# Kernel tuning notes

Hardware: AMD Instinct MI355X
Metric: run time of the kernel (lower is better)

The kernel has to match this reference:

```python
import jax, jax.numpy as jnp
import numpy as np

B, S, D, H = 2, 2048, 1024, 16
DH = D // H
DFF = 4 * D
EPS = 1e-5


def layernorm(x, g, b):
    mu = jnp.mean(x, axis=-1, keepdims=True)
    var = jnp.mean(jnp.square(x - mu), axis=-1, keepdims=True)
    return (x - mu) * jax.lax.rsqrt(var + EPS) * g + b


def setup_inputs() -> dict:
    key = jax.random.key(0)
    ks = jax.random.split(key, 12)
    s = 0.02
    return {
        "x": jax.random.normal(ks[0], (B, S, D), dtype=jnp.float32),
        "ln1_g": jnp.ones((D,), jnp.float32),
        "ln1_b": jnp.zeros((D,), jnp.float32),
        "Wq": jax.random.normal(ks[1], (D, D), jnp.float32) * s,
        "bq": jnp.zeros((D,), jnp.float32),
        "Wk": jax.random.normal(ks[2], (D, D), jnp.float32) * s,
        "bk": jnp.zeros((D,), jnp.float32),
        "Wv": jax.random.normal(ks[3], (D, D), jnp.float32) * s,
        "bv": jnp.zeros((D,), jnp.float32),
        "Wo": jax.random.normal(ks[4], (D, D), jnp.float32) * s,
        "bo": jnp.zeros((D,), jnp.float32),
        "ln2_g": jnp.ones((D,), jnp.float32),
        "ln2_b": jnp.zeros((D,), jnp.float32),
        "W1": jax.random.normal(ks[5], (D, DFF), jnp.float32) * s,
        "b1": jnp.zeros((DFF,), jnp.float32),
        "W2": jax.random.normal(ks[6], (DFF, D), jnp.float32) * s,
        "b2": jnp.zeros((D,), jnp.float32),
    }


def block(x, ln1_g, ln1_b, Wq, bq, Wk, bk, Wv, bv, Wo, bo, ln2_g, ln2_b, W1, b1, W2, b2):
    h = layernorm(x, ln1_g, ln1_b)
    # projections -> [B, H, S, DH]
    q = (h @ Wq + bq).reshape(B, S, H, DH).transpose(0, 2, 1, 3)
    k = (h @ Wk + bk).reshape(B, S, H, DH).transpose(0, 2, 1, 3)
    v = (h @ Wv + bv).reshape(B, S, H, DH).transpose(0, 2, 1, 3)
    scores = jnp.einsum('bhqd,bhkd->bhqk', q, k) / jnp.sqrt(jnp.float32(DH))
    causal = jnp.tril(jnp.ones((S, S), dtype=bool))  # True = keep
    scores = jnp.where(causal, scores, -jnp.inf)
    attn = jax.nn.softmax(scores, axis=-1)
    out = jnp.einsum('bhqk,bhkd->bhqd', attn, v)
    out = out.transpose(0, 2, 1, 3).reshape(B, S, D)
    x = x + out @ Wo + bo
    h2 = layernorm(x, ln2_g, ln2_b)
    ff = jax.nn.gelu(h2 @ W1 + b1, approximate=False) @ W2 + b2
    return x + ff


def reference(x, ln1_g, ln1_b, Wq, bq, Wk, bk, Wv, bv, Wo, bo, ln2_g, ln2_b, W1, b1, W2, b2):
    return block(x, ln1_g, ln1_b, Wq, bq, Wk, bk, Wv, bv, Wo, bo, ln2_g, ln2_b, W1, b1, W2, b2)
```

## Files before the change

### kernel.cpp

```cpp
#include <hip/hip_runtime.h>
#include <cstdint>
#include <cstddef>


#define DEV static __device__ __forceinline__

typedef unsigned short u16;
typedef __bf16 bf16x8 __attribute__((ext_vector_type(8)));
typedef u16    u16x8  __attribute__((ext_vector_type(8)));
typedef u16    u16x4  __attribute__((ext_vector_type(4)));
typedef float  f32x4  __attribute__((ext_vector_type(4)));

#define AEXP2(x) __builtin_amdgcn_exp2f(x)

DEV u16 f2bf(float f) {
  unsigned u = __builtin_bit_cast(unsigned, f);
  u += 0x7fffu + ((u >> 16) & 1u);
  return (u16)(u >> 16);
}
DEV u16 f2bfh(float f) {
  return __builtin_bit_cast(u16, (__bf16)f);
}

DEV void gl16(const void* g, void* l) {
  __builtin_amdgcn_global_load_lds(
      (const __attribute__((address_space(1))) unsigned*)g,
      (__attribute__((address_space(3))) unsigned*)l, 16, 0, 0);
}

__global__ __launch_bounds__(256)
void tconv(const float* __restrict__ in, u16* __restrict__ out, int R, int C)
{
  __shared__ float tile[32][33];
  const int tx = threadIdx.x & 31, ty = threadIdx.x >> 5;
  const int r0 = blockIdx.y * 32, c0 = blockIdx.x * 32;
#pragma unroll
  for (int i = 0; i < 4; ++i)
    tile[ty + 8*i][tx] = in[(size_t)(r0 + ty + 8*i) * C + c0 + tx];
  __syncthreads();
#pragma unroll
  for (int i = 0; i < 4; ++i)
    out[(size_t)(c0 + ty + 8*i) * R + r0 + tx] = f2bfh(tile[tx][ty + 8*i]);
}

__global__ __launch_bounds__(256)
void tconv4(const float* __restrict__ w0, const float* __restrict__ w1,
            const float* __restrict__ w2, const float* __restrict__ w3,
            u16* __restrict__ q0, u16* __restrict__ q1,
            u16* __restrict__ q2, u16* __restrict__ q3)
{
  __shared__ float tile[32][33];
  const int z = blockIdx.z;
  const float* in = z == 0 ? w0 : z == 1 ? w1 : z == 2 ? w2 : w3;
  u16* out       = z == 0 ? q0 : z == 1 ? q1 : z == 2 ? q2 : q3;
  const int tx = threadIdx.x & 31, ty = threadIdx.x >> 5;
  const int r0 = blockIdx.y * 32, c0 = blockIdx.x * 32;
#pragma unroll
  for (int i = 0; i < 4; ++i)
    tile[ty + 8*i][tx] = in[(size_t)(r0 + ty + 8*i) * 1024 + c0 + tx];
  __syncthreads();
#pragma unroll
  for (int i = 0; i < 4; ++i)
    out[(size_t)(c0 + ty + 8*i) * 1024 + r0 + tx] = f2bfh(tile[tx][ty + 8*i]);
}

__global__ __launch_bounds__(256)
void ln_fwd(const float* __restrict__ x, const float* __restrict__ g,
            const float* __restrict__ b, u16* __restrict__ out)
{
  const int row = blockIdx.x, t = threadIdx.x;
  const float4 v = ((const float4*)(x + (size_t)row * 1024))[t];
  float s1 = v.x + v.y + v.z + v.w;
  float s2 = v.x*v.x + v.y*v.y + v.z*v.z + v.w*v.w;
#pragma unroll
  for (int d = 1; d < 64; d <<= 1) {
    s1 += __shfl_xor(s1, d, 64);
    s2 += __shfl_xor(s2, d, 64);
  }
  __shared__ float sh[8];
  const int w = t >> 6;
  if ((t & 63) == 0) { sh[w] = s1; sh[w + 4] = s2; }
  __syncthreads();
  s1 = sh[0] + sh[1] + sh[2] + sh[3];
  s2 = sh[4] + sh[5] + sh[6] + sh[7];
  const float mu  = s1 * (1.0f / 1024.0f);
  const float var = s2 * (1.0f / 1024.0f) - mu * mu;
  const float rs  = rsqrtf(var + 1e-5f);
  const float4 gv = ((const float4*)g)[t];
  const float4 bv = ((const float4*)b)[t];
  u16x4 o;
  o[0] = f2bfh((v.x - mu) * rs * gv.x + bv.x);
  o[1] = f2bfh((v.y - mu) * rs * gv.y + bv.y);
  o[2] = f2bfh((v.z - mu) * rs * gv.z + bv.z);
  o[3] = f2bfh((v.w - mu) * rs * gv.w + bv.w);
  *(u16x4*)(out + (size_t)row * 1024 + t * 4) = o;
}

#define EPI_QKV  0
#define EPI_RES  1
#define EPI_GELU 2

#define QSCALE 0.180421f

template<int EPI, int BM, int PIPE, int CM>
__global__ __launch_bounds__(256)
void gemm_bt(const u16* __restrict__ A, const u16* __restrict__ Bt,
             const float* __restrict__ b0, const float* __restrict__ b1,
             const float* __restrict__ b2, const float* __restrict__ res,
             float* __restrict__ outf, u16* __restrict__ o0,
             u16* __restrict__ o1, u16* __restrict__ o2,
             int N, int K)
{
  constexpr int MI = BM / 32;
  constexpr int RA = BM / 32;
  constexpr int NB = PIPE == 2 ? 3 : (PIPE == 1 ? 2 : 1);
  static_assert(PIPE != 2 || BM == 64,  "vmcnt(6) assumes 6 loads/step");
  static_assert(PIPE != 1 || BM == 128, "vmcnt(8) assumes 8 loads/step");
  __shared__ u16 As[NB][BM * 64];
  __shared__ u16 Bs[NB][128 * 64];
  const int t = threadIdx.x, lane = t & 63, w = t >> 6;
  const int wr = w >> 1, wc = w & 1;
  const int d = blockIdx.x + gridDim.x * blockIdx.y;
  const int rr = d >> 3;
  const int m0 = ((d & 7) * CM + rr % CM) * BM;
  const int n0 = (rr / CM) * 128;
  const int li = lane & 15, lg = lane >> 4;

  const int srow = t >> 3;
  const int schunk = (t & 7) ^ (srow & 7);
  const u16* Ag = A  + (size_t)(m0 + srow) * K + schunk * 8;
  const u16* Bg = Bt + (size_t)(n0 + srow) * K + schunk * 8;

  auto STG = [&](int k0, int b) {
#pragma unroll
    for (int p = 0; p < RA; ++p)
      gl16(Ag + k0 + (size_t)(p * 32) * K, &As[b][t * 8 + p * 2048]);
#pragma unroll
    for (int p = 0; p < 4; ++p)
      gl16(Bg + k0 + (size_t)(p * 32) * K, &Bs[b][t * 8 + p * 2048]);
  };

  f32x4 acc[MI][4] = {};
  const int swz = (li & 7) << 4;

  auto COMPUTE = [&](int cur) {
#pragma unroll
    for (int ks = 0; ks < 2; ++ks) {
      bf16x8 af[MI], bfr[4];
#pragma unroll
      for (int i = 0; i < MI; ++i) {
        const int Ra = wr * (MI * 16) + i * 16 + li;
        af[i] = *(const bf16x8*)((const char*)As[cur] + Ra * 128 +
                                 ((ks * 64 + lg * 16) ^ swz));
      }
#pragma unroll
      for (int i = 0; i < 4; ++i) {
        const int Rb = wc * 64 + i * 16 + li;
        bfr[i] = *(const bf16x8*)((const char*)Bs[cur] + Rb * 128 +
                                  ((ks * 64 + lg * 16) ^ swz));
      }
#pragma unroll
      for (int mi = 0; mi < MI; ++mi)
#pragma unroll
        for (int ni = 0; ni < 4; ++ni)
          acc[mi][ni] = __builtin_amdgcn_mfma_f32_16x16x32_bf16(
              af[mi], bfr[ni], acc[mi][ni], 0, 0, 0);
    }
  };

  if (PIPE == 2) {
    STG(0, 0);
    if (64 < K) STG(64, 1);
    int cur = 0;
    for (int k0 = 0; k0 < K; k0 += 64) {
      if (k0 + 64 < K)
        asm volatile("s_waitcnt vmcnt(6)" ::: "memory");
      else
        asm volatile("s_waitcnt vmcnt(0)" ::: "memory");
      __builtin_amdgcn_s_barrier();
      __builtin_amdgcn_sched_barrier(0);
      COMPUTE(cur);
      if (k0 + 128 < K) {
        int nxt = cur + 2; if (nxt >= 3) nxt -= 3;
        STG(k0 + 128, nxt);
      }
      cur = (cur + 1 == 3) ? 0 : cur + 1;
    }
  } else if (PIPE == 1) {
    STG(0, 0);
    for (int k0 = 0; k0 < K; k0 += 64) {
      const int cur = (k0 >> 6) & 1;
      if (k0 + 64 < K) {
        STG(k0 + 64, cur ^ 1);
        asm volatile("s_waitcnt vmcnt(8)" ::: "memory");
      } else {
        asm volatile("s_waitcnt vmcnt(0)" ::: "memory");
      }
      __builtin_amdgcn_s_barrier();
      __builtin_amdgcn_sched_barrier(0);
      COMPUTE(cur);
      __builtin_amdgcn_sched_barrier(0);
      __builtin_amdgcn_s_barrier();
    }
  } else {
    for (int k0 = 0; k0 < K; k0 += 64) {
      __syncthreads();
      STG(k0, 0);
      __syncthreads();
      COMPUTE(0);
    }
  }

  const int crow = wr * (MI * 16) + lg * 4;
  const int ccol = wc * 64 + li;

  if (EPI == EPI_QKV) {
    const int which = n0 >> 10;
    const float* bias = which == 0 ? b0 : which == 1 ? b1 : b2;
    const int nn0 = n0 & 1023;
    if (which == 2) {
#pragma unroll
      for (int mi = 0; mi < MI; ++mi)
#pragma unroll
        for (int ni = 0; ni < 4; ++ni) {
          const int gm0 = m0 + crow + mi * 16;
          const int b_ = gm0 >> 11, s_ = gm0 & 2047;
          const int gc = nn0 + ccol + ni * 16;
          const int h_ = gc >> 6, d_ = gc & 63;
          u16x4 pk;
#pragma unroll
          for (int r = 0; r < 4; ++r) pk[r] = f2bfh(acc[mi][ni][r] + bias[gc]);
          *(u16x4*)(o2 + ((size_t)(b_ * 16 + h_) * 64 + d_) * 2048 + s_) = pk;
        }
    } else {
      u16* outp = which == 0 ? o0 : o1;
      const float sc = which == 0 ? QSCALE : 1.0f;
#pragma unroll
      for (int mi = 0; mi < MI; ++mi)
#pragma unroll
        for (int ni = 0; ni < 4; ++ni)
#pragma unroll
          for (int r = 0; r < 4; ++r) {
            const int gm = m0 + crow + mi * 16 + r;
            const int gc = nn0 + ccol + ni * 16;
            const float v = (acc[mi][ni][r] + bias[gc]) * sc;
            const int b_ = gm >> 11, s_ = gm & 2047;
            const int h_ = gc >> 6,  d_ = gc & 63;
            outp[((size_t)(b_ * 16 + h_) * 2048 + s_) * 64 + d_] = f2bfh(v);
          }
    }
  } else {
#pragma unroll
    for (int mi = 0; mi < MI; ++mi)
#pragma unroll
      for (int ni = 0; ni < 4; ++ni)
#pragma unroll
        for (int r = 0; r < 4; ++r) {
          const int gm = m0 + crow + mi * 16 + r;
          const int gn = n0 + ccol + ni * 16;
          const float v = acc[mi][ni][r] + b0[gn];
          if (EPI == EPI_RES) {
            const size_t o = (size_t)gm * N + gn;
            outf[o] = v + res[o];
          } else {
            const float y = 0.7978845608f * (v + 0.044715f * v * v * v);
            const float e = AEXP2(fminf(y * 2.8853900818f, 80.0f));
            const float gl = v * e * __builtin_amdgcn_rcpf(e + 1.0f);
            o0[(size_t)gm * N + gn] = f2bfh(gl);
          }
        }
  }
}

__global__ __launch_bounds__(512, 4)
void attn_fwd(const u16* __restrict__ qb, const u16* __restrict__ kb,
              const u16* __restrict__ vtb, u16* __restrict__ ob)
{
  __shared__ u16 Ks[2][128 * 64];
  __shared__ u16 Vt[2][64 * 128];
  __shared__ u16 Ps[8][16 * 64];
  const int t = threadIdx.x, w = t >> 6, lane = t & 63;
  const int li = lane & 15, lg = lane >> 4;
  const int bh = blockIdx.y;
  const int bx = blockIdx.x;
  const int qt = (bh & 16) ? (15 - bx) : bx;
  const int q0 = qt * 128;

  const size_t qrow = (size_t)bh * 2048 + q0 + w * 16 + li;
  const bf16x8 aq0 = *(const bf16x8*)(qb + qrow * 64 + lg * 8);
  const bf16x8 aq1 = *(const bf16x8*)(qb + qrow * 64 + lg * 8 + 32);

  f32x4 o[4] = {};
  float mrun[4], lrun[4];
#pragma unroll
  for (int r = 0; r < 4; ++r) { mrun[r] = -1e30f; lrun[r] = 0.0f; }

  const u16* kbase = kb  + (size_t)bh * 2048 * 64;
  const u16* vbase = vtb + (size_t)bh * 64 * 2048;
  const int ntile = qt + 1;

  const int kchunk = (t & 7)  ^ ((t >> 3) & 7);
  const int vchunk = (t & 15) ^ ((t >> 4) & 15);
  const u16* kg = kbase + (size_t)(t >> 3) * 64 + kchunk * 8;
  const u16* vg = vbase + (size_t)(t >> 4) * 2048 + vchunk * 8;

#define STAGE(tk_, b_)                                              \
  {                                                                 \
    const int kv0s = (tk_) * 128;                                   \
    gl16(kg + (size_t)kv0s * 64,        &Ks[b_][t * 8]);            \
    gl16(kg + (size_t)(kv0s + 64) * 64, &Ks[b_][t * 8 + 4096]);     \
    gl16(vg + kv0s,                     &Vt[b_][t * 8]);            \
    gl16(vg + kv0s + (size_t)32 * 2048, &Vt[b_][t * 8 + 4096]);     \
  }

  STAGE(0, 0);
  __syncthreads();

  for (int tk = 0; tk < ntile; ++tk) {
    const int cur = tk & 1;
    const int kv0 = tk * 128;
    if (tk + 1 < ntile) STAGE(tk + 1, 1 - cur);

    f32x4 s[8];
    __builtin_amdgcn_s_setprio(1);
#pragma unroll
    for (int cf = 0; cf < 8; ++cf) {
      const int row = cf * 16 + li;
      const char* kc = (const char*)Ks[cur] + row * 128;
      const int sw = (row & 7) << 4;
      const bf16x8 bk0 = *(const bf16x8*)(kc + ((lg * 16)      ^ sw));
      const bf16x8 bk1 = *(const bf16x8*)(kc + ((lg * 16 + 64) ^ sw));
      f32x4 z = {};
      z = __builtin_amdgcn_mfma_f32_16x16x32_bf16(aq0, bk0, z, 0, 0, 0);
      z = __builtin_amdgcn_mfma_f32_16x16x32_bf16(aq1, bk1, z, 0, 0, 0);
      s[cf] = z;
    }
    __builtin_amdgcn_s_setprio(0);
    const int row0 = q0 + w * 16 + lg * 4;
    if (tk == ntile - 1) {
#pragma unroll
      for (int cf = 0; cf < 8; ++cf)
#pragma unroll
        for (int r = 0; r < 4; ++r)
          if (kv0 + cf * 16 + li > row0 + r) s[cf][r] = -1e30f;
    }

    float pmax[4];
#pragma unroll
    for (int r = 0; r < 4; ++r) {
      const float a = fmaxf(fmaxf(s[0][r], s[1][r]), fmaxf(s[2][r], s[3][r]));
      const float b = fmaxf(fmaxf(s[4][r], s[5][r]), fmaxf(s[6][r], s[7][r]));
      pmax[r] = fmaxf(a, b);
    }
    bool need = false;
#pragma unroll
    for (int r = 0; r < 4; ++r) need = need || (pmax[r] > mrun[r] + 11.5f);
    if (__any((int)need)) {
#pragma unroll
      for (int d = 1; d < 16; d <<= 1)
#pragma unroll
        for (int r = 0; r < 4; ++r)
          pmax[r] = fmaxf(pmax[r], __shfl_xor(pmax[r], d, 64));
#pragma unroll
      for (int r = 0; r < 4; ++r) {
        const float mnew = fmaxf(mrun[r], pmax[r]);
        const float scl  = AEXP2(mrun[r] - mnew);
        lrun[r] *= scl;
#pragma unroll
        for (int n = 0; n < 4; ++n) o[n][r] *= scl;
        mrun[r] = mnew;
      }
    }
#pragma unroll
    for (int cf = 0; cf < 8; ++cf)
#pragma unroll
      for (int r = 0; r < 4; ++r) {
        const float pv = AEXP2(s[cf][r] - mrun[r]);
        s[cf][r] = pv;
        lrun[r] += pv;
      }

#pragma unroll
    for (int kh = 0; kh < 2; ++kh) {
#pragma unroll
      for (int cf2 = 0; cf2 < 4; ++cf2)
#pragma unroll
        for (int r = 0; r < 4; ++r) {
          const int prow = lg * 4 + r;
          const int pcolB = (cf2 * 16 + li) * 2;
          *(u16*)((char*)Ps[w] + prow * 128 + (pcolB ^ ((prow & 7) << 4))) =
              f2bfh(s[kh * 4 + cf2][r]);
        }
      __builtin_amdgcn_s_setprio(1);
#pragma unroll
      for (int ks = 0; ks < 2; ++ks) {
        const char* pc = (const char*)Ps[w] + li * 128;
        const bf16x8 ap =
            *(const bf16x8*)(pc + ((lg * 16 + ks * 64) ^ ((li & 7) << 4)));
#pragma unroll
        for (int n = 0; n < 4; ++n) {
          const int vrow = n * 16 + li;
          const char* vc = (const char*)Vt[cur] + vrow * 256;
          const int colB = lg * 16 + ks * 64 + kh * 128;
          const bf16x8 bv =
              *(const bf16x8*)(vc + (colB ^ ((vrow & 15) << 4)));
          o[n] = __builtin_amdgcn_mfma_f32_16x16x32_bf16(ap, bv, o[n], 0, 0, 0);
        }
      }
      __builtin_amdgcn_s_setprio(0);
    }

    __syncthreads();
  }
#undef STAGE

#pragma unroll
  for (int d = 1; d < 16; d <<= 1)
#pragma unroll
    for (int r = 0; r < 4; ++r)
      lrun[r] += __shfl_xor(lrun[r], d, 64);

  float inv[4];
#pragma unroll
  for (int r = 0; r < 4; ++r) inv[r] = __builtin_amdgcn_rcpf(lrun[r]);
  const int b_ = bh >> 4, h_ = bh & 15;
#pragma unroll
  for (int n = 0; n < 4; ++n)
#pragma unroll
    for (int r = 0; r < 4; ++r) {
      const int rowg = q0 + w * 16 + lg * 4 + r;
      ob[((size_t)b_ * 2048 + rowg) * 1024 + h_ * 64 + n * 16 + li] =
          f2bfh(o[n][r] * inv[r]);
    }
}

extern "C" void kernel_launch(void* const* d_in, const int* in_sizes, int n_in,
                              void* d_out, int out_size, void* d_ws, size_t ws_size,
                              hipStream_t stream) {
  const float* x    = (const float*)d_in[0];
  const float* ln1g = (const float*)d_in[1];
  const float* ln1b = (const float*)d_in[2];
  const float* Wq   = (const float*)d_in[3];
  const float* bq   = (const float*)d_in[4];
  const float* Wk   = (const float*)d_in[5];
  const float* bk   = (const float*)d_in[6];
  const float* Wv   = (const float*)d_in[7];
  const float* bv   = (const float*)d_in[8];
  const float* Wo   = (const float*)d_in[9];
  const float* bo   = (const float*)d_in[10];
  const float* ln2g = (const float*)d_in[11];
  const float* ln2b = (const float*)d_in[12];
  const float* W1   = (const float*)d_in[13];
  const float* b1   = (const float*)d_in[14];
  const float* W2   = (const float*)d_in[15];
  const float* b2   = (const float*)d_in[16];

  char* ws = (char*)d_ws;
  const size_t MB = 1u << 20;
  u16*   hb   = (u16*)(ws + 0);
  u16*   Wqt  = (u16*)(ws + 8  * MB);
  u16*   Wkt  = (u16*)(ws + 10 * MB);
  u16*   Wvt  = (u16*)(ws + 12 * MB);
  u16*   Wot  = (u16*)(ws + 14 * MB);
  u16*   W1t  = (u16*)(ws + 16 * MB);
  u16*   W2t  = (u16*)(ws + 24 * MB);
  u16*   qbuf = (u16*)(ws + 32 * MB);
  u16*   kbuf = (u16*)(ws + 40 * MB);
  u16*   aob  = (u16*)(ws + 48 * MB);
  u16*   vtb  = (u16*)(ws + 56 * MB);
  float* x2   = (float*)(ws + 64 * MB);
  u16*   h2   = hb;
  u16*   ff1  = qbuf;

  const dim3 blk(256);
  tconv4<<<dim3(32, 32, 4), blk, 0, stream>>>(Wq, Wk, Wv, Wo, Wqt, Wkt, Wvt, Wot);
  tconv<<<dim3(128, 32), blk, 0, stream>>>(W1, W1t, 1024, 4096);
  tconv<<<dim3(32, 128), blk, 0, stream>>>(W2, W2t, 4096, 1024);

  ln_fwd<<<4096, blk, 0, stream>>>(x, ln1g, ln1b, hb);

  gemm_bt<EPI_QKV, 128, 1, 4><<<dim3(24, 32), blk, 0, stream>>>(
      hb, Wqt, bq, bk, bv, nullptr, nullptr, qbuf, kbuf, vtb, 3072, 1024);

  attn_fwd<<<dim3(16, 32), dim3(512), 0, stream>>>(qbuf, kbuf, vtb, aob);

  gemm_bt<EPI_RES, 64, 2, 8><<<dim3(8, 64), blk, 0, stream>>>(
      aob, Wot, bo, nullptr, nullptr, x, x2, nullptr, nullptr, nullptr, 1024, 1024);

  ln_fwd<<<4096, blk, 0, stream>>>(x2, ln2g, ln2b, h2);

  gemm_bt<EPI_GELU, 128, 1, 4><<<dim3(32, 32), blk, 0, stream>>>(
      h2, W1t, b1, nullptr, nullptr, nullptr, nullptr, ff1, nullptr, nullptr, 4096, 1024);

  gemm_bt<EPI_RES, 64, 2, 8><<<dim3(8, 64), blk, 0, stream>>>(
      ff1, W2t, b2, nullptr, nullptr, x2, (float*)d_out, nullptr, nullptr, nullptr, 1024, 4096);
}
```

Baseline: 215.7 us.

## Use 256x256 tiles with 512-thread blocks for QKV and FFN1 GEMMs

Adds a gemm256 kernel that gives each 512-thread block a 256x256 output tile, so each of 8 waves holds a 128x64 accumulator. It replaces the 128x128 tiled GEMM for the QKV projection and the first FFN GEMM. The larger tile raises arithmetic intensity and cuts global/LDS traffic per FLOP. The cost is heavy register pressure, 128KB of LDS, and far fewer blocks (192 and 256) for the GPU's 256 CUs, which may leave some CUs idle or unbalanced.

```diff
diff --git a/kernel.cpp b/kernel.cpp
--- a/kernel.cpp
+++ b/kernel.cpp
@@ -13,11 +13,6 @@
 
 #define AEXP2(x) __builtin_amdgcn_exp2f(x)
 
-DEV u16 f2bf(float f) {
-  unsigned u = __builtin_bit_cast(unsigned, f);
-  u += 0x7fffu + ((u >> 16) & 1u);
-  return (u16)(u >> 16);
-}
 DEV u16 f2bfh(float f) {
   return __builtin_bit_cast(u16, (__bf16)f);
 }
@@ -102,28 +97,22 @@
 
 #define QSCALE 0.180421f
 
-template<int EPI, int BM, int PIPE, int CM>
-__global__ __launch_bounds__(256)
-void gemm_bt(const u16* __restrict__ A, const u16* __restrict__ Bt,
+template<int EPI>
+__global__ __launch_bounds__(512, 2)
+void gemm256(const u16* __restrict__ A, const u16* __restrict__ Bt,
              const float* __restrict__ b0, const float* __restrict__ b1,
-             const float* __restrict__ b2, const float* __restrict__ res,
-             float* __restrict__ outf, u16* __restrict__ o0,
-             u16* __restrict__ o1, u16* __restrict__ o2,
+             const float* __restrict__ b2,
+             u16* __restrict__ o0, u16* __restrict__ o1, u16* __restrict__ o2,
              int N, int K)
 {
-  constexpr int MI = BM / 32;
-  constexpr int RA = BM / 32;
-  constexpr int NB = PIPE == 2 ? 3 : (PIPE == 1 ? 2 : 1);
-  static_assert(PIPE != 2 || BM == 64,  "vmcnt(6) assumes 6 loads/step");
-  static_assert(PIPE != 1 || BM == 128, "vmcnt(8) assumes 8 loads/step");
-  __shared__ u16 As[NB][BM * 64];
-  __shared__ u16 Bs[NB][128 * 64];
+  __shared__ u16 As[2][256 * 64];
+  __shared__ u16 Bs[2][256 * 64];
   const int t = threadIdx.x, lane = t & 63, w = t >> 6;
-  const int wr = w >> 1, wc = w & 1;
+  const int wr = w >> 2, wc = w & 3;
   const int d = blockIdx.x + gridDim.x * blockIdx.y;
   const int rr = d >> 3;
-  const int m0 = ((d & 7) * CM + rr % CM) * BM;
-  const int n0 = (rr / CM) * 128;
+  const int m0 = ((d & 7) * 2 + (rr & 1)) * 256;
+  const int n0 = (rr >> 1) * 256;
   const int li = lane & 15, lg = lane >> 4;
 
   const int srow = t >> 3;
@@ -133,23 +122,23 @@
 
   auto STG = [&](int k0, int b) {
 #pragma unroll
-    for (int p = 0; p < RA; ++p)
-      gl16(Ag + k0 + (size_t)(p * 32) * K, &As[b][t * 8 + p * 2048]);
-#pragma unroll
     for (int p = 0; p < 4; ++p)
-      gl16(Bg + k0 + (size_t)(p * 32) * K, &Bs[b][t * 8 + p * 2048]);
+      gl16(Ag + k0 + (size_t)(p * 64) * K, &As[b][t * 8 + p * 4096]);
+#pragma unroll
+    for (int p = 0; p < 4; ++p)
+      gl16(Bg + k0 + (size_t)(p * 64) * K, &Bs[b][t * 8 + p * 4096]);
   };
 
-  f32x4 acc[MI][4] = {};
+  f32x4 acc[8][4] = {};
   const int swz = (li & 7) << 4;
 
   auto COMPUTE = [&](int cur) {
 #pragma unroll
     for (int ks = 0; ks < 2; ++ks) {
-      bf16x8 af[MI], bfr[4];
-#pragma unroll
-      for (int i = 0; i < MI; ++i) {
-        const int Ra = wr * (MI * 16) + i * 16 + li;
+      bf16x8 af[8], bfr[4];
+#pragma unroll
+      for (int i = 0; i < 8; ++i) {
+        const int Ra = wr * 128 + i * 16 + li;
         af[i] = *(const bf16x8*)((const char*)As[cur] + Ra * 128 +
                                  ((ks * 64 + lg * 16) ^ swz));
       }
@@ -160,7 +149,7 @@
                                   ((ks * 64 + lg * 16) ^ swz));
       }
 #pragma unroll
-      for (int mi = 0; mi < MI; ++mi)
+      for (int mi = 0; mi < 8; ++mi)
 #pragma unroll
         for (int ni = 0; ni < 4; ++ni)
           acc[mi][ni] = __builtin_amdgcn_mfma_f32_16x16x32_bf16(
@@ -168,50 +157,23 @@
     }
   };
 
-  if (PIPE == 2) {
-    STG(0, 0);
-    if (64 < K) STG(64, 1);
-    int cur = 0;
-    for (int k0 = 0; k0 < K; k0 += 64) {
-      if (k0 + 64 < K)
-        asm volatile("s_waitcnt vmcnt(6)" ::: "memory");
-      else
-        asm volatile("s_waitcnt vmcnt(0)" ::: "memory");
-      __builtin_amdgcn_s_barrier();
-      __builtin_amdgcn_sched_barrier(0);
-      COMPUTE(cur);
-      if (k0 + 128 < K) {
-        int nxt = cur + 2; if (nxt >= 3) nxt -= 3;
-        STG(k0 + 128, nxt);
-      }
-      cur = (cur + 1 == 3) ? 0 : cur + 1;
-    }
-  } else if (PIPE == 1) {
-    STG(0, 0);
-    for (int k0 = 0; k0 < K; k0 += 64) {
-      const int cur = (k0 >> 6) & 1;
-      if (k0 + 64 < K) {
-        STG(k0 + 64, cur ^ 1);
-        asm volatile("s_waitcnt vmcnt(8)" ::: "memory");
-      } else {
-        asm volatile("s_waitcnt vmcnt(0)" ::: "memory");
-      }
-      __builtin_amdgcn_s_barrier();
-      __builtin_amdgcn_sched_barrier(0);
-      COMPUTE(cur);
-      __builtin_amdgcn_sched_barrier(0);
-      __builtin_amdgcn_s_barrier();
-    }
-  } else {
-    for (int k0 = 0; k0 < K; k0 += 64) {
-      __syncthreads();
-      STG(k0, 0);
-      __syncthreads();
-      COMPUTE(0);
-    }
+  STG(0, 0);
+  for (int k0 = 0; k0 < K; k0 += 64) {
+    const int cur = (k0 >> 6) & 1;
+    if (k0 + 64 < K) {
+      STG(k0 + 64, cur ^ 1);
+      asm volatile("s_waitcnt vmcnt(8)" ::: "memory");
+    } else {
+      asm volatile("s_waitcnt vmcnt(0)" ::: "memory");
+    }
+    __builtin_amdgcn_s_barrier();
+    __builtin_amdgcn_sched_barrier(0);
+    COMPUTE(cur);
+    __builtin_amdgcn_sched_barrier(0);
+    __builtin_amdgcn_s_barrier();
   }
 
-  const int crow = wr * (MI * 16) + lg * 4;
+  const int crow = wr * 128 + lg * 4;
   const int ccol = wc * 64 + li;
 
   if (EPI == EPI_QKV) {
@@ -220,7 +182,7 @@
     const int nn0 = n0 & 1023;
     if (which == 2) {
 #pragma unroll
-      for (int mi = 0; mi < MI; ++mi)
+      for (int mi = 0; mi < 8; ++mi)
 #pragma unroll
         for (int ni = 0; ni < 4; ++ni) {
           const int gm0 = m0 + crow + mi * 16;
@@ -236,7 +198,7 @@
       u16* outp = which == 0 ? o0 : o1;
       const float sc = which == 0 ? QSCALE : 1.0f;
 #pragma unroll
-      for (int mi = 0; mi < MI; ++mi)
+      for (int mi = 0; mi < 8; ++mi)
 #pragma unroll
         for (int ni = 0; ni < 4; ++ni)
 #pragma unroll
@@ -251,7 +213,7 @@
     }
   } else {
 #pragma unroll
-    for (int mi = 0; mi < MI; ++mi)
+    for (int mi = 0; mi < 8; ++mi)
 #pragma unroll
       for (int ni = 0; ni < 4; ++ni)
 #pragma unroll
@@ -259,17 +221,108 @@
           const int gm = m0 + crow + mi * 16 + r;
           const int gn = n0 + ccol + ni * 16;
           const float v = acc[mi][ni][r] + b0[gn];
-          if (EPI == EPI_RES) {
-            const size_t o = (size_t)gm * N + gn;
-            outf[o] = v + res[o];
-          } else {
-            const float y = 0.7978845608f * (v + 0.044715f * v * v * v);
-            const float e = AEXP2(fminf(y * 2.8853900818f, 80.0f));
-            const float gl = v * e * __builtin_amdgcn_rcpf(e + 1.0f);
-            o0[(size_t)gm * N + gn] = f2bfh(gl);
-          }
+          const float y = 0.7978845608f * (v + 0.044715f * v * v * v);
+          const float e = AEXP2(fminf(y * 2.8853900818f, 80.0f));
+          const float gl = v * e * __builtin_amdgcn_rcpf(e + 1.0f);
+          o0[(size_t)gm * N + gn] = f2bfh(gl);
         }
   }
+}
+
+template<int EPI, int BM, int CM>
+__global__ __launch_bounds__(256)
+void gemm_bt(const u16* __restrict__ A, const u16* __restrict__ Bt,
+             const float* __restrict__ b0, const float* __restrict__ res,
+             float* __restrict__ outf, u16* __restrict__ o0,
+             int N, int K)
+{
+  constexpr int MI = BM / 32;
+  constexpr int RA = BM / 32;
+  static_assert(BM == 64, "vmcnt(6) assumes 6 loads/step");
+  __shared__ u16 As[3][BM * 64];
+  __shared__ u16 Bs[3][128 * 64];
+  const int t = threadIdx.x, lane = t & 63, w = t >> 6;
+  const int wr = w >> 1, wc = w & 1;
+  const int d = blockIdx.x + gridDim.x * blockIdx.y;
+  const int rr = d >> 3;
+  const int m0 = ((d & 7) * CM + rr % CM) * BM;
+  const int n0 = (rr / CM) * 128;
+  const int li = lane & 15, lg = lane >> 4;
+
+  const int srow = t >> 3;
+  const int schunk = (t & 7) ^ (srow & 7);
+  const u16* Ag = A  + (size_t)(m0 + srow) * K + schunk * 8;
+  const u16* Bg = Bt + (size_t)(n0 + srow) * K + schunk * 8;
+
+  auto STG = [&](int k0, int b) {
+#pragma unroll
+    for (int p = 0; p < RA; ++p)
+      gl16(Ag + k0 + (size_t)(p * 32) * K, &As[b][t * 8 + p * 2048]);
+#pragma unroll
+    for (int p = 0; p < 4; ++p)
+      gl16(Bg + k0 + (size_t)(p * 32) * K, &Bs[b][t * 8 + p * 2048]);
+  };
+
+  f32x4 acc[MI][4] = {};
+  const int swz = (li & 7) << 4;
+
+  auto COMPUTE = [&](int cur) {
+#pragma unroll
+    for (int ks = 0; ks < 2; ++ks) {
+      bf16x8 af[MI], bfr[4];
+#pragma unroll
+      for (int i = 0; i < MI; ++i) {
+        const int Ra = wr * (MI * 16) + i * 16 + li;
+        af[i] = *(const bf16x8*)((const char*)As[cur] + Ra * 128 +
+                                 ((ks * 64 + lg * 16) ^ swz));
+      }
+#pragma unroll
+      for (int i = 0; i < 4; ++i) {
+        const int Rb = wc * 64 + i * 16 + li;
+        bfr[i] = *(const bf16x8*)((const char*)Bs[cur] + Rb * 128 +
+                                  ((ks * 64 + lg * 16) ^ swz));
+      }
+#pragma unroll
+      for (int mi = 0; mi < MI; ++mi)
+#pragma unroll
+        for (int ni = 0; ni < 4; ++ni)
+          acc[mi][ni] = __builtin_amdgcn_mfma_f32_16x16x32_bf16(
+              af[mi], bfr[ni], acc[mi][ni], 0, 0, 0);
+    }
+  };
+
+  STG(0, 0);
+  if (64 < K) STG(64, 1);
+  int cur = 0;
+  for (int k0 = 0; k0 < K; k0 += 64) {
+    if (k0 + 64 < K)
+      asm volatile("s_waitcnt vmcnt(6)" ::: "memory");
+    else
+      asm volatile("s_waitcnt vmcnt(0)" ::: "memory");
+    __builtin_amdgcn_s_barrier();
+    __builtin_amdgcn_sched_barrier(0);
+    COMPUTE(cur);
+    if (k0 + 128 < K) {
+      int nxt = cur + 2; if (nxt >= 3) nxt -= 3;
+      STG(k0 + 128, nxt);
+    }
+    cur = (cur + 1 == 3) ? 0 : cur + 1;
+  }
+
+  const int crow = wr * (MI * 16) + lg * 4;
+  const int ccol = wc * 64 + li;
+#pragma unroll
+  for (int mi = 0; mi < MI; ++mi)
+#pragma unroll
+    for (int ni = 0; ni < 4; ++ni)
+#pragma unroll
+      for (int r = 0; r < 4; ++r) {
+        const int gm = m0 + crow + mi * 16 + r;
+        const int gn = n0 + ccol + ni * 16;
+        const float v = acc[mi][ni][r] + b0[gn];
+        const size_t o = (size_t)gm * N + gn;
+        outf[o] = v + res[o];
+      }
 }
 
 __global__ __launch_bounds__(512, 4)
@@ -479,19 +532,19 @@
 
   ln_fwd<<<4096, blk, 0, stream>>>(x, ln1g, ln1b, hb);
 
-  gemm_bt<EPI_QKV, 128, 1, 4><<<dim3(24, 32), blk, 0, stream>>>(
-      hb, Wqt, bq, bk, bv, nullptr, nullptr, qbuf, kbuf, vtb, 3072, 1024);
+  gemm256<EPI_QKV><<<dim3(12, 16), dim3(512), 0, stream>>>(
+      hb, Wqt, bq, bk, bv, qbuf, kbuf, vtb, 3072, 1024);
 
   attn_fwd<<<dim3(16, 32), dim3(512), 0, stream>>>(qbuf, kbuf, vtb, aob);
 
-  gemm_bt<EPI_RES, 64, 2, 8><<<dim3(8, 64), blk, 0, stream>>>(
-      aob, Wot, bo, nullptr, nullptr, x, x2, nullptr, nullptr, nullptr, 1024, 1024);
+  gemm_bt<EPI_RES, 64, 8><<<dim3(8, 64), blk, 0, stream>>>(
+      aob, Wot, bo, x, x2, nullptr, 1024, 1024);
 
   ln_fwd<<<4096, blk, 0, stream>>>(x2, ln2g, ln2b, h2);
 
-  gemm_bt<EPI_GELU, 128, 1, 4><<<dim3(32, 32), blk, 0, stream>>>(
-      h2, W1t, b1, nullptr, nullptr, nullptr, nullptr, ff1, nullptr, nullptr, 4096, 1024);
-
-  gemm_bt<EPI_RES, 64, 2, 8><<<dim3(8, 64), blk, 0, stream>>>(
-      ff1, W2t, b2, nullptr, nullptr, x2, (float*)d_out, nullptr, nullptr, nullptr, 1024, 4096);
-}
+  gemm256<EPI_GELU><<<dim3(16, 16), dim3(512), 0, stream>>>(
+      h2, W1t, b1, nullptr, nullptr, ff1, nullptr, nullptr, 4096, 1024);
+
+  gemm_bt<EPI_RES, 64, 8><<<dim3(8, 64), blk, 0, stream>>>(
+      ff1, W2t, b2, x2, (float*)d_out, nullptr, 1024, 4096);
+}
```

New measurement: 214.4 us. Within noise of the previous version (-0.6%).
